# Kernel tuning notes

Measured on AMD Instinct MI355X. Metric: run time of the kernel, lower is better.

## Reference

```python
import jax, jax.numpy as jnp
import numpy as np

D_MODEL = 2048
D_STATE = 64
D_CONV = 4
EXPAND = 2
HEADDIM = 64
NGROUPS = 1
CHUNK = 64
D_INNER = EXPAND * D_MODEL            # 4096
NHEADS = D_INNER // HEADDIM           # 64
D_XBC = D_INNER + 2 * NGROUPS * D_STATE
D_IN_PROJ = 2 * D_INNER + 2 * NGROUPS * D_STATE + NHEADS


def setup_inputs():
    key = jax.random.key(0)
    ks = jax.random.split(key, 8)
    B, L = 2, 4096
    u = jax.random.normal(ks[0], (B, L, D_MODEL), jnp.float32)
    W_in = jax.random.normal(ks[1], (D_IN_PROJ, D_MODEL), jnp.float32) * 0.02
    conv_w = jax.random.normal(ks[2], (D_XBC, D_CONV), jnp.float32) * 0.2
    conv_b = jnp.zeros((D_XBC,), jnp.float32)
    dt = jnp.exp(jax.random.uniform(ks[3], (NHEADS,)) * (np.log(0.1) - np.log(0.001)) + np.log(0.001))
    dt = jnp.clip(dt, 1e-4)
    dt_bias = dt + jnp.log(-jnp.expm1(-dt))
    A_log = jnp.log(jax.random.uniform(ks[4], (NHEADS,), minval=1.0, maxval=16.0))
    D_param = jnp.ones((NHEADS,), jnp.float32)
    norm_w = jnp.ones((D_INNER,), jnp.float32)
    W_out = jax.random.normal(ks[5], (D_MODEL, D_INNER), jnp.float32) * 0.02
    return dict(u=u, W_in=W_in, conv_w=conv_w, conv_b=conv_b, dt_bias=dt_bias,
                A_log=A_log, D_param=D_param, norm_w=norm_w, W_out=W_out)


def segsum(x):
    # x: (..., T) -> (..., T, T) with entry [l,s] = sum_{s< i <= l} x[i], -inf above diag
    T = x.shape[-1]
    mask_strict = jnp.tril(jnp.ones((T, T), bool), k=-1)
    mask_incl = jnp.tril(jnp.ones((T, T), bool), k=0)
    xe = jnp.where(mask_strict, x[..., :, None], 0.0)  # element [l,s] = x[l] if l>s
    xseg = jnp.cumsum(xe, axis=-2)
    return jnp.where(mask_incl, xseg, -jnp.inf)


def ssd_scan(X, A, Bm, Cm, block_len=CHUNK):
    # X: (b,L,h,p), A: (b,L,h), Bm/Cm: (b,L,h,n)
    b, seqlen, h, p = X.shape
    n = Bm.shape[-1]
    pad_len = (block_len - seqlen % block_len) % block_len
    if pad_len > 0:
        X = jnp.pad(X, ((0, 0), (0, pad_len), (0, 0), (0, 0)))
        A = jnp.pad(A, ((0, 0), (0, pad_len), (0, 0)))
        Bm = jnp.pad(Bm, ((0, 0), (0, pad_len), (0, 0), (0, 0)))
        Cm = jnp.pad(Cm, ((0, 0), (0, pad_len), (0, 0), (0, 0)))
    L = X.shape[1]
    c = L // block_len
    Xc = X.reshape(b, c, block_len, h, p)
    Ac = A.reshape(b, c, block_len, h).transpose(0, 3, 1, 2)  # (b,h,c,l)
    Bc = Bm.reshape(b, c, block_len, h, n)
    Cc = Cm.reshape(b, c, block_len, h, n)
    A_cum = jnp.cumsum(Ac, axis=-1)                           # (b,h,c,l)
    Lmat = jnp.exp(segsum(Ac))                                # (b,h,c,l,s)
    CB = jnp.einsum('bclhn,bcshn->bhcls', Cc, Bc)
    Y_diag = jnp.einsum('bhcls,bcshp->bhclp', CB * Lmat, Xc)
    decay_states = jnp.exp(A_cum[..., -1:] - A_cum)           # (b,h,c,l)
    states = jnp.einsum('bhcl,bclhn,bclhp->bhcpn', decay_states, Bc, Xc)
    init = jnp.zeros((b, h, 1, p, n), X.dtype)
    states = jnp.concatenate([init, states], axis=2)          # (b,h,c+1,p,n)
    chunk_decay = jnp.pad(A_cum[..., -1], ((0, 0), (0, 0), (1, 0)))  # (b,h,c+1)
    decay_chunk = jnp.exp(segsum(chunk_decay))                # (b,h,c+1,c+1)
    new_states = jnp.einsum('bhzc,bhcpn->bhzpn', decay_chunk, states)[:, :, :-1]
    Y_off = jnp.einsum('bclhn,bhcpn,bhcl->bhclp', Cc, new_states, jnp.exp(A_cum))
    Y = (Y_diag + Y_off).transpose(0, 2, 3, 1, 4).reshape(b, L, h, p)
    if pad_len > 0:
        Y = Y[:, :seqlen]
    return Y


def rmsnorm_grouped(x, w, ngroups, eps=1e-5):
    gs = x.shape[-1] // ngroups
    xg = x.reshape(*x.shape[:-1], ngroups, gs)
    xg = xg * jax.lax.rsqrt(jnp.mean(xg * xg, axis=-1, keepdims=True) + eps)
    return xg.reshape(x.shape) * w


def reference(u, W_in, conv_w, conv_b, dt_bias, A_log, D_param, norm_w, W_out):
    B, L, _ = u.shape
    zxbcdt = u @ W_in.T                                      # (B,L,d_in_proj)
    z = zxbcdt[..., :D_INNER]
    xBC = zxbcdt[..., D_INNER:D_INNER + D_XBC]
    dt = zxbcdt[..., D_INNER + D_XBC:]
    # causal depthwise conv1d, kernel D_CONV, left-pad D_CONV-1
    xpad = jnp.pad(xBC, ((0, 0), (D_CONV - 1, 0), (0, 0)))
    conv = conv_b
    for k in range(D_CONV):
        conv = conv + conv_w[:, k] * xpad[:, k:k + L, :]
    xBC = jax.nn.silu(conv)
    x = xBC[..., :D_INNER].reshape(B, L, NHEADS, HEADDIM)
    B_ssm = xBC[..., D_INNER:D_INNER + NGROUPS * D_STATE].reshape(B, L, NGROUPS, D_STATE)
    C_ssm = xBC[..., D_INNER + NGROUPS * D_STATE:].reshape(B, L, NGROUPS, D_STATE)
    if NGROUPS < NHEADS:
        rep = NHEADS // NGROUPS
        B_ssm = jnp.repeat(B_ssm, rep, axis=2)
        C_ssm = jnp.repeat(C_ssm, rep, axis=2)
    dt = jax.nn.softplus(dt + dt_bias)                        # (B,L,nheads)
    A = -jnp.exp(A_log)                                       # (nheads,)
    y = ssd_scan(x * dt[..., None], A * dt, B_ssm, C_ssm, block_len=CHUNK)
    y = y + D_param[:, None] * x
    y = y.reshape(B, L, D_INNER)
    y = rmsnorm_grouped(y * jax.nn.silu(z), norm_w, NGROUPS)
    return y @ W_out.T
```

## Files before the change

kernel.cpp:

```cpp
#include <hip/hip_runtime.h>
#include <hip/hip_bf16.h>
#include <math.h>

#define SEQ       4096
#define DMODEL    2048
#define DINNER    4096
#define DXBC      4224
#define NPROJ     8384
#define NHEADS    64
#define HDIM      64
#define DSTATE    64
#define NCHUNK    64
#define XLD       4352

typedef __attribute__((ext_vector_type(8))) _Float16 half8;
typedef __attribute__((ext_vector_type(2))) _Float16 half2v;
typedef __attribute__((ext_vector_type(4))) float floatx4;

__device__ __forceinline__ void async_copy16(void* lds, const void* g) {
  __builtin_amdgcn_global_load_lds(
      (const __attribute__((address_space(1))) unsigned int*)g,
      (__attribute__((address_space(3))) unsigned int*)lds, 16, 0, 0);
}

__device__ __forceinline__ float silu_f(float x) { return x / (1.f + __expf(-x)); }

__device__ __forceinline__ void cvt8(const float* __restrict__ s, _Float16* __restrict__ d) {
  float4 a = *(const float4*)s;
  float4 b = *(const float4*)(s + 4);
  half8 h;
  h[0] = (_Float16)a.x; h[1] = (_Float16)a.y; h[2] = (_Float16)a.z; h[3] = (_Float16)a.w;
  h[4] = (_Float16)b.x; h[5] = (_Float16)b.y; h[6] = (_Float16)b.z; h[7] = (_Float16)b.w;
  *(half8*)d = h;
}

__global__ void diag_kernel(float* out, float v) { out[0] = v; }

__global__ void cvt8_kernel(const float* __restrict__ src, _Float16* __restrict__ dst, int n8) {
  int i = blockIdx.x * 256 + threadIdx.x;
  if (i < n8) cvt8(src + (size_t)i * 8, dst + (size_t)i * 8);
}

#define U_N8 (SEQ * DMODEL / 8)
__global__ void cvt_in_kernel(const float* __restrict__ u, const float* __restrict__ W_in,
                              _Float16* __restrict__ ubf, _Float16* __restrict__ winbf) {
  int i = blockIdx.x * 256 + threadIdx.x;
  if (i < U_N8) {
    cvt8(u + (size_t)i * 8, ubf + (size_t)i * 8);
  } else {
    int j = i - U_N8;
    int row = j >> 8;
    size_t off = (size_t)j * 8;
    if (row < NPROJ) {
      cvt8(W_in + off, winbf + off);
    } else {
      half8 zz = {};
      *(half8*)(winbf + off) = zz;
    }
  }
}

template <typename OT>
__global__ __launch_bounds__(256) void gemm_bt64(
    const _Float16* __restrict__ A, const _Float16* __restrict__ B,
    OT* __restrict__ C0, OT* __restrict__ C1, int K,
    int ldc0, int ldc1, int ncol0, int tiles_m, int tiles_n) {
  __shared__ __align__(16) _Float16 As[128 * 64];
  __shared__ __align__(16) _Float16 Bs[128 * 64];
  int t = threadIdx.x;
  int nt = tiles_m * tiles_n;
  int id = blockIdx.x;
  int id2 = ((nt & 7) == 0) ? ((id & 7) * (nt >> 3) + (id >> 3)) : id;
  int wband = tiles_m << 2;
  int g = id2 / wband;
  int rm = id2 - g * wband;
  int bw = tiles_n - (g << 2); if (bw > 4) bw = 4;
  int pn = (g << 2) + rm % bw;
  int pm = rm / bw;
  int m0 = pm * 128, n0 = pn * 128;

  int w = t >> 6, lane = t & 63, q = lane >> 4, r = lane & 15;
  int wm = (w >> 1) * 64, wn = (w & 1) * 64;
  int rowoff = lane >> 3;
  int chunkoff = ((lane & 7) ^ rowoff) * 8;
  const _Float16* gA[4];
  const _Float16* gB[4];
#pragma unroll
  for (int i = 0; i < 4; ++i) {
    gA[i] = A + (size_t)(m0 + i * 32 + w * 8 + rowoff) * K + chunkoff;
    gB[i] = B + (size_t)(n0 + i * 32 + w * 8 + rowoff) * K + chunkoff;
  }
  floatx4 acc[4][4] = {};
  for (int k0 = 0; k0 < K; k0 += 64) {
#pragma unroll
    for (int i = 0; i < 4; ++i) {
      async_copy16(As + (i * 32 + w * 8) * 64, gA[i] + k0);
      async_copy16(Bs + (i * 32 + w * 8) * 64, gB[i] + k0);
    }
    __syncthreads();
#pragma unroll
    for (int kk = 0; kk < 64; kk += 32) {
      half8 af[4], bf[4];
#pragma unroll
      for (int im = 0; im < 4; ++im) {
        int R = wm + im * 16 + r;
        af[im] = *(const half8*)&As[R * 64 + ((((kk >> 3) + q) ^ (R & 7)) << 3)];
      }
#pragma unroll
      for (int in = 0; in < 4; ++in) {
        int R = wn + in * 16 + r;
        bf[in] = *(const half8*)&Bs[R * 64 + ((((kk >> 3) + q) ^ (R & 7)) << 3)];
      }
#pragma unroll
      for (int im = 0; im < 4; ++im)
#pragma unroll
        for (int in = 0; in < 4; ++in)
          acc[im][in] =
              __builtin_amdgcn_mfma_f32_16x16x32_f16(af[im], bf[in], acc[im][in], 0, 0, 0);
    }
    __syncthreads();
  }
  OT* Cp = (n0 < ncol0) ? C0 : C1;
  int ldc = (n0 < ncol0) ? ldc0 : ldc1;
  int cb = (n0 < ncol0) ? n0 : n0 - ncol0;
#pragma unroll
  for (int im = 0; im < 4; ++im)
#pragma unroll
    for (int in = 0; in < 4; ++in)
#pragma unroll
      for (int i = 0; i < 4; ++i)
        Cp[(size_t)(m0 + wm + im * 16 + q * 4 + i) * ldc + cb + wn + in * 16 + r] =
            (OT)acc[im][in][i];
}

template <typename OT>
__global__ __launch_bounds__(512, 2) void gemm256(
    const _Float16* __restrict__ A, const _Float16* __restrict__ B,
    OT* __restrict__ C, int K, int ldc, int tiles_m, int tiles_n) {
  __shared__ __align__(16) _Float16 As[2][2][128 * 64];
  __shared__ __align__(16) _Float16 Bs[2][2][128 * 64];
  int t = threadIdx.x;
  int nwg = tiles_m * tiles_n;
  int id = blockIdx.x;
  int wgid = ((nwg & 7) == 0) ? ((id & 7) * (nwg >> 3) + (id >> 3)) : id;
  int wband = tiles_m << 2;
  int g = wgid / wband;
  int rm = wgid - g * wband;
  int bw = tiles_n - (g << 2); if (bw > 4) bw = 4;
  int pn = (g << 2) + rm % bw;
  int pm = rm / bw;
  int m0 = pm * 256, n0 = pn * 256;

  int w = t >> 6, lane = t & 63, q4 = lane >> 4, r16 = lane & 15;
  int srow = lane >> 3;
  int schunk = ((lane & 7) ^ srow) << 3;
  const _Float16* gAb = A + (size_t)(m0 + w * 8 + srow) * K + schunk;
  const _Float16* gBb = B + (size_t)(n0 + w * 8 + srow) * K + schunk;
  int Ra = (w >> 2) * 64 + r16;
  int Rb = (w & 3) * 32 + r16;

  floatx4 acc[4][4][2] = {};
  half8 af[4][2], bf[2][2];

#define STAGE_A(buf_, H_, kt_)                                                 \
  {                                                                            \
    _Pragma("unroll") for (int i_ = 0; i_ < 2; ++i_)                           \
        async_copy16(&As[buf_][H_][(i_ * 64 + w * 8) * 64],                    \
                     gAb + (size_t)((H_)*128 + i_ * 64) * K + ((kt_) << 6));   \
  }
#define STAGE_B(buf_, H_, kt_)                                                 \
  {                                                                            \
    _Pragma("unroll") for (int i_ = 0; i_ < 2; ++i_)                           \
        async_copy16(&Bs[buf_][H_][(i_ * 64 + w * 8) * 64],                    \
                     gBb + (size_t)((H_)*128 + i_ * 64) * K + ((kt_) << 6));   \
  }
#define LDA(half_)                                                             \
  _Pragma("unroll") for (int m_ = 0; m_ < 4; ++m_)                             \
  _Pragma("unroll") for (int k_ = 0; k_ < 2; ++k_) {                           \
    int R_ = Ra + m_ * 16;                                                     \
    af[m_][k_] = *(const half8*)&As[cur][half_]                                \
        [R_ * 64 + (((k_ * 4 + q4) ^ (R_ & 7)) << 3)];                         \
  }
#define LDB(half_)                                                             \
  _Pragma("unroll") for (int n_ = 0; n_ < 2; ++n_)                             \
  _Pragma("unroll") for (int k_ = 0; k_ < 2; ++k_) {                           \
    int R_ = Rb + n_ * 16;                                                     \
    bf[n_][k_] = *(const half8*)&Bs[cur][half_]                                \
        [R_ * 64 + (((k_ * 4 + q4) ^ (R_ & 7)) << 3)];                         \
  }
#define MM(sq_)                                                                \
  __builtin_amdgcn_s_setprio(1);                                               \
  _Pragma("unroll") for (int m_ = 0; m_ < 4; ++m_)                             \
  _Pragma("unroll") for (int n_ = 0; n_ < 2; ++n_)                             \
  _Pragma("unroll") for (int k_ = 0; k_ < 2; ++k_)                             \
      acc[sq_][m_][n_] = __builtin_amdgcn_mfma_f32_16x16x32_f16(               \
          af[m_][k_], bf[n_][k_], acc[sq_][m_][n_], 0, 0, 0);                  \
  __builtin_amdgcn_s_setprio(0);
#define BARF() { __builtin_amdgcn_s_barrier(); asm volatile("" ::: "memory"); }
#define WAITLGKM()                                                             \
  {                                                                            \
    asm volatile("s_waitcnt lgkmcnt(0)" ::: "memory");                         \
    __builtin_amdgcn_sched_barrier(0);                                         \
  }

  int NT = K >> 6;
  STAGE_A(0, 0, 0);
  STAGE_B(0, 0, 0);
  STAGE_B(0, 1, 0);
  STAGE_A(0, 1, 0);
  asm volatile("s_waitcnt vmcnt(2)" ::: "memory");
  BARF();

  for (int kt = 0; kt < NT; ++kt) {
    int cur = kt & 1, nxt = cur ^ 1;
    bool more = (kt + 1 < NT);
    LDA(0);
    LDB(0);
    if (more) STAGE_A(nxt, 0, kt + 1);
    BARF();
    WAITLGKM();
    MM(0);
    BARF();
    LDB(1);
    if (more) {
      STAGE_B(nxt, 0, kt + 1);
      asm volatile("s_waitcnt vmcnt(4)" ::: "memory");
    } else {
      asm volatile("s_waitcnt vmcnt(0)" ::: "memory");
    }
    BARF();
    WAITLGKM();
    MM(1);
    BARF();
    LDA(1);
    if (more) STAGE_B(nxt, 1, kt + 1);
    BARF();
    WAITLGKM();
    MM(2);
    BARF();
    LDB(0);
    if (more) {
      STAGE_A(nxt, 1, kt + 1);
      asm volatile("s_waitcnt vmcnt(2)" ::: "memory");
    }
    BARF();
    WAITLGKM();
    MM(3);
    BARF();
  }

  const int paC[4] = {0, 0, 1, 1};
  const int pbC[4] = {0, 1, 1, 0};
#pragma unroll
  for (int sq = 0; sq < 4; ++sq) {
    int rb = m0 + paC[sq] * 128 + (w >> 2) * 64 + q4 * 4;
    int cb = n0 + pbC[sq] * 128 + (w & 3) * 32 + r16;
#pragma unroll
    for (int m = 0; m < 4; ++m)
#pragma unroll
      for (int n = 0; n < 2; ++n)
#pragma unroll
        for (int i = 0; i < 4; ++i)
          C[(size_t)(rb + m * 16 + i) * ldc + cb + n * 16] = (OT)acc[sq][m][n][i];
  }
#undef STAGE_A
#undef STAGE_B
#undef LDA
#undef LDB
#undef MM
#undef BARF
#undef WAITLGKM
}

#define CONVB (SEQ * (DXBC / 2) / 256)
__global__ __launch_bounds__(256) void conv_dtscan_kernel(
    const _Float16* __restrict__ xin, const float* __restrict__ conv_w,
    const float* __restrict__ conv_b, _Float16* __restrict__ xcv,
    const float* __restrict__ dt_bias, const float* __restrict__ A_log,
    float* __restrict__ dtp, float* __restrict__ acum, float* __restrict__ chs) {
  int t = threadIdx.x;
  if (blockIdx.x < CONVB) {
    int idx = blockIdx.x * 256 + t;
    int l = idx / (DXBC / 2);
    int c = (idx - l * (DXBC / 2)) * 2;
    const _Float16* zc = xin + (size_t)l * XLD + c;
    float a0 = conv_b[c], a1 = conv_b[c + 1];
#pragma unroll
    for (int k = 0; k < 4; ++k) {
      int off = k - 3;
      if (l + off >= 0) {
        half2v v = *(const half2v*)(zc + (long)off * XLD);
        a0 += conv_w[c * 4 + k] * (float)v[0];
        a1 += conv_w[c * 4 + 4 + k] * (float)v[1];
      }
    }
    half2v o;
    o[0] = (_Float16)silu_f(a0);
    o[1] = (_Float16)silu_f(a1);
    *(half2v*)(xcv + (size_t)l * DXBC + c) = o;
  } else {
    __shared__ float dAs[64 * 65];
    int c = blockIdx.x - CONVB;
    int h = t & 63;
    const _Float16* dtraw = xin + DXBC;
    float bias = dt_bias[h];
    float negA = -__expf(A_log[h]);
#pragma unroll
    for (int i = 0; i < 16; ++i) {
      int l = i * 4 + (t >> 6);
      int row = c * 64 + l;
      float x = (float)dtraw[(size_t)row * XLD + h] + bias;
      float dtv = (x > 20.f) ? x : log1pf(__expf(x));
      dtp[(size_t)row * 64 + h] = dtv;
      dAs[l * 65 + h] = negA * dtv;
    }
    __syncthreads();
    if (t < 64) {
      float a = 0.f;
      size_t base = ((size_t)c * 64 + t) * 64;
      for (int l = 0; l < 64; ++l) {
        a += dAs[l * 65 + t];
        acum[base + l] = a;
      }
      chs[c * 64 + t] = a;
    }
  }
}

__global__ __launch_bounds__(256) void states_kernel(
    const _Float16* __restrict__ xcv, const float* __restrict__ dtp,
    const float* __restrict__ acum, const float* __restrict__ chs,
    _Float16* __restrict__ states) {
  int bid = blockIdx.x;
  int c = bid & 63, h = bid >> 6;
  int row0 = c * 64;
  int acbase = (c * 64 + h) * 64;
  __shared__ __align__(16) _Float16 XdT[64 * 72];
  __shared__ __align__(16) _Float16 BdT[64 * 72];
  __shared__ float dec[64];
  int t = threadIdx.x;
  if (t < 64) dec[t] = __expf(chs[acbase >> 6] - acum[acbase + t]);
  __syncthreads();
#pragma unroll
  for (int i = 0; i < 16; ++i) {
    int flat = i * 256 + t;
    int l = flat >> 6, col = flat & 63;
    int grow = row0 + l;
    float dtv = dtp[(size_t)grow * 64 + h];
    float xv = (float)xcv[(size_t)grow * DXBC + h * 64 + col] * dtv;
    XdT[col * 72 + l] = (_Float16)xv;
    float bv = (float)xcv[(size_t)grow * DXBC + DINNER + col] * dec[l];
    BdT[col * 72 + l] = (_Float16)bv;
  }
  __syncthreads();
  int w = t >> 6, lane = t & 63, q = lane >> 4, r = lane & 15;
#pragma unroll
  for (int in = 0; in < 4; ++in) {
    floatx4 a4 = {0.f, 0.f, 0.f, 0.f};
#pragma unroll
    for (int k0 = 0; k0 < 64; k0 += 32) {
      half8 af = *(const half8*)&XdT[(w * 16 + r) * 72 + k0 + q * 8];
      half8 bf = *(const half8*)&BdT[(in * 16 + r) * 72 + k0 + q * 8];
      a4 = __builtin_amdgcn_mfma_f32_16x16x32_f16(af, bf, a4, 0, 0, 0);
    }
#pragma unroll
    for (int i = 0; i < 4; ++i)
      states[((size_t)bid * 64 + (w * 16 + q * 4 + i)) * 64 + in * 16 + r] = (_Float16)a4[i];
  }
}

__global__ __launch_bounds__(256) void scan_kernel(_Float16* __restrict__ states,
                                                   const float* __restrict__ chs) {
  int bid = blockIdx.x;
  int h = bid >> 4, seg = bid & 15;
  size_t base = ((size_t)h * 64) * 4096 + seg * 256 + threadIdx.x;
  float carry = 0.f;
  float s_cur = (float)states[base];
  for (int c = 0; c < 64; ++c) {
    size_t idx = base + (size_t)c * 4096;
    float s_next = (c < 63) ? (float)states[idx + 4096] : 0.f;
    float ec = __expf(chs[c * 64 + h]);
    states[idx] = (_Float16)carry;
    carry = carry * ec + s_cur;
    s_cur = s_next;
  }
}

__global__ __launch_bounds__(256) void yout_kernel(
    const _Float16* __restrict__ xcv, const float* __restrict__ dtp,
    const float* __restrict__ acum, const _Float16* __restrict__ sin_,
    const float* __restrict__ Dp, _Float16* __restrict__ Y) {
  int bid = blockIdx.x;
  int c = bid & 63, h = bid >> 6;
  int row0 = c * 64;
  int acbase = (c * 64 + h) * 64;
  __shared__ __align__(16) _Float16 Cs[64 * 72];
  __shared__ __align__(16) _Float16 Bt[64 * 72];
  __shared__ __align__(16) _Float16 XdT[64 * 72];
  __shared__ __align__(16) _Float16 Ms[64 * 72];
  __shared__ float acs[64];
  int t = threadIdx.x;
  if (t < 64) acs[t] = acum[acbase + t];
#pragma unroll
  for (int i = 0; i < 16; ++i) {
    int flat = i * 256 + t;
    int l = flat >> 6, col = flat & 63;
    int grow = row0 + l;
    const _Float16* rp = xcv + (size_t)grow * DXBC;
    Cs[l * 72 + col] = rp[DINNER + DSTATE + col];
    Bt[l * 72 + col] = rp[DINNER + col];
    float xv = (float)rp[h * 64 + col] * dtp[(size_t)grow * 64 + h];
    XdT[col * 72 + l] = (_Float16)xv;
  }
  __syncthreads();
  int w = t >> 6, lane = t & 63, q = lane >> 4, r = lane & 15;
  int m = w * 16 + r;
#pragma unroll
  for (int in = 0; in < 4; ++in) {
    floatx4 cb = {0.f, 0.f, 0.f, 0.f};
#pragma unroll
    for (int k0 = 0; k0 < 64; k0 += 32) {
      half8 af = *(const half8*)&Cs[m * 72 + k0 + q * 8];
      half8 bf = *(const half8*)&Bt[(in * 16 + r) * 72 + k0 + q * 8];
      cb = __builtin_amdgcn_mfma_f32_16x16x32_f16(af, bf, cb, 0, 0, 0);
    }
#pragma unroll
    for (int i = 0; i < 4; ++i) {
      int l = w * 16 + q * 4 + i;
      int s = in * 16 + r;
      float v = (s <= l) ? cb[i] * __expf(acs[l] - acs[s]) : 0.f;
      Ms[l * 72 + s] = (_Float16)v;
    }
  }
  __syncthreads();
  size_t sbase = (size_t)bid * 4096;
  float Dh = Dp[h];
#pragma unroll
  for (int in = 0; in < 4; ++in) {
    floatx4 acc = {0.f, 0.f, 0.f, 0.f};
#pragma unroll
    for (int k0 = 0; k0 < 64; k0 += 32) {
      half8 af = *(const half8*)&Cs[m * 72 + k0 + q * 8];
      half8 bf = *(const half8*)&sin_[sbase + (size_t)(in * 16 + r) * 64 + k0 + q * 8];
      acc = __builtin_amdgcn_mfma_f32_16x16x32_f16(af, bf, acc, 0, 0, 0);
    }
#pragma unroll
    for (int i = 0; i < 4; ++i) acc[i] *= __expf(acs[w * 16 + q * 4 + i]);
#pragma unroll
    for (int k0 = 0; k0 < 64; k0 += 32) {
      half8 af = *(const half8*)&Ms[m * 72 + k0 + q * 8];
      half8 bf = *(const half8*)&XdT[(in * 16 + r) * 72 + k0 + q * 8];
      acc = __builtin_amdgcn_mfma_f32_16x16x32_f16(af, bf, acc, 0, 0, 0);
    }
#pragma unroll
    for (int i = 0; i < 4; ++i) {
      int l = w * 16 + q * 4 + i;
      int p = in * 16 + r;
      int grow = row0 + l;
      float xv = (float)xcv[(size_t)grow * DXBC + h * 64 + p];
      Y[(size_t)grow * DINNER + h * 64 + p] = (_Float16)(acc[i] + Dh * xv);
    }
  }
}

__global__ __launch_bounds__(256) void rmsnorm_kernel(const _Float16* __restrict__ Y,
                                                      _Float16* __restrict__ Z,
                                                      const float* __restrict__ norm_w) {
  int row = blockIdx.x;
  const half8* y8 = (const half8*)(Y + (size_t)row * DINNER);
  half8* z8 = (half8*)(Z + (size_t)row * DINNER);
  __shared__ float red[4];
  int t = threadIdx.x;
  float g[16];
  float ss = 0.f;
#pragma unroll
  for (int i = 0; i < 2; ++i) {
    int j = i * 256 + t;
    half8 yv = y8[j];
    half8 zv = z8[j];
#pragma unroll
    for (int e = 0; e < 8; ++e) {
      float gv = (float)yv[e] * silu_f((float)zv[e]);
      g[i * 8 + e] = gv;
      ss += gv * gv;
    }
  }
#pragma unroll
  for (int o = 32; o > 0; o >>= 1) ss += __shfl_down(ss, o, 64);
  if ((t & 63) == 0) red[t >> 6] = ss;
  __syncthreads();
  float rs = rsqrtf((red[0] + red[1] + red[2] + red[3]) / (float)DINNER + 1e-5f);
#pragma unroll
  for (int i = 0; i < 2; ++i) {
    int j = i * 256 + t;
    const float4* w4 = (const float4*)(norm_w + j * 8);
    float4 wa = w4[0], wb = w4[1];
    half8 o;
    o[0] = (_Float16)(g[i * 8 + 0] * rs * wa.x);
    o[1] = (_Float16)(g[i * 8 + 1] * rs * wa.y);
    o[2] = (_Float16)(g[i * 8 + 2] * rs * wa.z);
    o[3] = (_Float16)(g[i * 8 + 3] * rs * wa.w);
    o[4] = (_Float16)(g[i * 8 + 4] * rs * wb.x);
    o[5] = (_Float16)(g[i * 8 + 5] * rs * wb.y);
    o[6] = (_Float16)(g[i * 8 + 6] * rs * wb.z);
    o[7] = (_Float16)(g[i * 8 + 7] * rs * wb.w);
    z8[j] = o;
  }
}

extern "C" void kernel_launch(void* const* d_in, const int* in_sizes, int n_in,
                              void* d_out, int out_size, void* d_ws, size_t ws_size,
                              hipStream_t stream) {
  const float* u       = (const float*)d_in[0];
  const float* W_in    = (const float*)d_in[1];
  const float* conv_w  = (const float*)d_in[2];
  const float* conv_b  = (const float*)d_in[3];
  const float* dt_bias = (const float*)d_in[4];
  const float* A_log   = (const float*)d_in[5];
  const float* D_param = (const float*)d_in[6];
  const float* norm_w  = (const float*)d_in[7];
  const float* W_out   = (const float*)d_in[8];
  float* out = (float*)d_out;
  char* ws = (char*)d_ws;

  const size_t NEED_MID   = 192954368ULL;
  const size_t NEED_SMALL = 140525568ULL;
  bool big = (ws_size >= NEED_MID);
  if (!big && ws_size < NEED_SMALL) {
    diag_kernel<<<1, 1, 0, stream>>>(out, (float)ws_size);
    return;
  }

  if (big) {
    _Float16* zb     = (_Float16*)(ws + 0);
    _Float16* xbcdtb = (_Float16*)(ws + 67108864ULL);
    _Float16* xcv    = (_Float16*)(ws + 102760448ULL);
    _Float16* winbf  = xcv;
    _Float16* states = (_Float16*)(ws + 137363456ULL);
    _Float16* ubf    = states;
    _Float16* woutbf = (_Float16*)(ws + 170917888ULL);
    float* dtp  = (float*)(ws + 187695104ULL);
    float* acum = (float*)(ws + 188743680ULL);
    float* chs  = (float*)(ws + 189792256ULL);

    cvt8_kernel<<<DMODEL * DINNER / 8 / 256, 256, 0, stream>>>(
        W_out, woutbf, DMODEL * DINNER / 8);

    for (int b = 0; b < 2; ++b) {
      const float* ub = u + (size_t)b * SEQ * DMODEL;
      _Float16* zbb = zb + (size_t)b * SEQ * DINNER;

      cvt_in_kernel<<<U_N8 / 256 + 8448, 256, 0, stream>>>(ub, W_in, ubf, winbf);

      gemm256<_Float16><<<256, 512, 0, stream>>>(ubf, winbf, zbb, DMODEL, DINNER, 16, 16);
      gemm_bt64<_Float16><<<32 * 34, 256, 0, stream>>>(
          ubf, winbf + (size_t)DINNER * DMODEL, xbcdtb, xbcdtb,
          DMODEL, XLD, XLD, 1 << 30, 32, 34);

      conv_dtscan_kernel<<<CONVB + NCHUNK, 256, 0, stream>>>(
          xbcdtb, conv_w, conv_b, xcv, dt_bias, A_log, dtp, acum, chs);

      states_kernel<<<NHEADS * NCHUNK, 256, 0, stream>>>(xcv, dtp, acum, chs, states);
      scan_kernel<<<NHEADS * 16, 256, 0, stream>>>(states, chs);
      yout_kernel<<<NHEADS * NCHUNK, 256, 0, stream>>>(xcv, dtp, acum, states, D_param,
                                                       xbcdtb );

      rmsnorm_kernel<<<SEQ, 256, 0, stream>>>(xbcdtb, zbb, norm_w);
    }

    gemm256<float><<<256, 512, 0, stream>>>(zb, woutbf, out, DINNER, DMODEL, 32, 8);
  } else {
    _Float16* zb     = (_Float16*)(ws + 0);
    _Float16* xbcdtb = (_Float16*)(ws + 33554432ULL);
    _Float16* Yb     = xbcdtb;
    _Float16* xcv    = (_Float16*)(ws + 69206016ULL);
    _Float16* winbf  = xcv;
    _Float16* states = (_Float16*)(ws + 103809024ULL);
    _Float16* ubf    = states;
    _Float16* woutbf = states;
    float* dtp  = (float*)(ws + 137363456ULL);
    float* acum = (float*)(ws + 139460608ULL);
    float* chs  = (float*)(ws + 140509184ULL);

    for (int b = 0; b < 2; ++b) {
      const float* ub = u + (size_t)b * SEQ * DMODEL;
      float* outb = out + (size_t)b * SEQ * DMODEL;

      cvt_in_kernel<<<U_N8 / 256 + 8448, 256, 0, stream>>>(ub, W_in, ubf, winbf);
      gemm_bt64<_Float16><<<32 * 66, 256, 0, stream>>>(
          ubf, winbf, zb, xbcdtb, DMODEL, DINNER, XLD, DINNER, 32, 66);
      conv_dtscan_kernel<<<CONVB + NCHUNK, 256, 0, stream>>>(
          xbcdtb, conv_w, conv_b, xcv, dt_bias, A_log, dtp, acum, chs);
      states_kernel<<<NHEADS * NCHUNK, 256, 0, stream>>>(xcv, dtp, acum, chs, states);
      scan_kernel<<<NHEADS * 16, 256, 0, stream>>>(states, chs);
      yout_kernel<<<NHEADS * NCHUNK, 256, 0, stream>>>(xcv, dtp, acum, states, D_param, Yb);
      rmsnorm_kernel<<<SEQ, 256, 0, stream>>>(Yb, zb, norm_w);
      cvt8_kernel<<<DMODEL * DINNER / 8 / 256, 256, 0, stream>>>(
          W_out, woutbf, DMODEL * DINNER / 8);
      gemm_bt64<float><<<32 * 16, 256, 0, stream>>>(
          zb, woutbf, outb, outb, DINNER, DMODEL, DMODEL, 1 << 30, 32, 16);
    }
  }
}
```

Before: 1.092 ms.

## Deepen gemm256 prefetch to two k-tiles and fold xBC projection into it

The 256x256 GEMM now stages loads two k-iterations ahead instead of one, reusing the current buffer once its sub-tiles have been consumed. Its vmcnt waits move to the end of each iteration. The kernel also gains a split output (C0/C1 by column), so the in-projection GEMM covers both the z columns and the first 4096 xBC columns in a single 512-workgroup launch. Only the small 128-column tail (B/C/dt) is left to the 64-tile kernel. The goal is to hide global-load latency better and to run most of the projection on the faster large-tile kernel, at the cost of more in-flight loads and subtler buffer-reuse hazards.

```diff
diff --git a/kernel.cpp b/kernel.cpp
--- a/kernel.cpp
+++ b/kernel.cpp
@@ -136,7 +136,8 @@
 template <typename OT>
 __global__ __launch_bounds__(512, 2) void gemm256(
     const _Float16* __restrict__ A, const _Float16* __restrict__ B,
-    OT* __restrict__ C, int K, int ldc, int tiles_m, int tiles_n) {
+    OT* __restrict__ C0, OT* __restrict__ C1, int K,
+    int ldc0, int ldc1, int ncol0, int tiles_m, int tiles_n) {
   __shared__ __align__(16) _Float16 As[2][2][128 * 64];
   __shared__ __align__(16) _Float16 Bs[2][2][128 * 64];
   int t = threadIdx.x;
@@ -205,63 +206,71 @@
 
   int NT = K >> 6;
   STAGE_A(0, 0, 0);
-  STAGE_B(0, 0, 0);
   STAGE_B(0, 1, 0);
   STAGE_A(0, 1, 0);
-  asm volatile("s_waitcnt vmcnt(2)" ::: "memory");
+  STAGE_B(0, 0, 0);
+  if (NT > 1) {
+    STAGE_A(1, 0, 1);
+    STAGE_B(1, 1, 1);
+    STAGE_A(1, 1, 1);
+    asm volatile("s_waitcnt vmcnt(6)" ::: "memory");
+  } else {
+    asm volatile("s_waitcnt vmcnt(0)" ::: "memory");
+  }
   BARF();
 
   for (int kt = 0; kt < NT; ++kt) {
     int cur = kt & 1, nxt = cur ^ 1;
-    bool more = (kt + 1 < NT);
     LDA(0);
     LDB(0);
-    if (more) STAGE_A(nxt, 0, kt + 1);
+    if (kt + 1 < NT) STAGE_B(nxt, 0, kt + 1);
     BARF();
     WAITLGKM();
     MM(0);
     BARF();
     LDB(1);
-    if (more) {
-      STAGE_B(nxt, 0, kt + 1);
-      asm volatile("s_waitcnt vmcnt(4)" ::: "memory");
-    } else {
-      asm volatile("s_waitcnt vmcnt(0)" ::: "memory");
-    }
+    if (kt + 2 < NT) STAGE_A(cur, 0, kt + 2);
     BARF();
     WAITLGKM();
     MM(1);
     BARF();
     LDA(1);
-    if (more) STAGE_B(nxt, 1, kt + 1);
+    if (kt + 2 < NT) STAGE_B(cur, 1, kt + 2);
     BARF();
     WAITLGKM();
     MM(2);
     BARF();
     LDB(0);
-    if (more) {
-      STAGE_A(nxt, 1, kt + 1);
-      asm volatile("s_waitcnt vmcnt(2)" ::: "memory");
-    }
+    if (kt + 2 < NT) STAGE_A(cur, 1, kt + 2);
     BARF();
     WAITLGKM();
     MM(3);
+    if (kt + 1 < NT) {
+      if (kt + 2 < NT) {
+        asm volatile("s_waitcnt vmcnt(6)" ::: "memory");
+      } else {
+        asm volatile("s_waitcnt vmcnt(0)" ::: "memory");
+      }
+    }
     BARF();
   }
 
   const int paC[4] = {0, 0, 1, 1};
   const int pbC[4] = {0, 1, 1, 0};
+  OT* Cp = (n0 < ncol0) ? C0 : C1;
+  int ldc = (n0 < ncol0) ? ldc0 : ldc1;
+  int cb0 = (n0 < ncol0) ? n0 : n0 - ncol0;
 #pragma unroll
   for (int sq = 0; sq < 4; ++sq) {
     int rb = m0 + paC[sq] * 128 + (w >> 2) * 64 + q4 * 4;
-    int cb = n0 + pbC[sq] * 128 + (w & 3) * 32 + r16;
+    int cb = cb0 + pbC[sq] * 128 + (w & 3) * 32 + r16;
 #pragma unroll
     for (int m = 0; m < 4; ++m)
 #pragma unroll
       for (int n = 0; n < 2; ++n)
 #pragma unroll
         for (int i = 0; i < 4; ++i)
-          C[(size_t)(rb + m * 16 + i) * ldc + cb + n * 16] = (OT)acc[sq][m][n][i];
+          Cp[(size_t)(rb + m * 16 + i) * ldc + cb + n * 16] = (OT)acc[sq][m][n][i];
   }
 #undef STAGE_A
 #undef STAGE_B
@@ -552,10 +561,11 @@
 
       cvt_in_kernel<<<U_N8 / 256 + 8448, 256, 0, stream>>>(ub, W_in, ubf, winbf);
 
-      gemm256<_Float16><<<256, 512, 0, stream>>>(ubf, winbf, zbb, DMODEL, DINNER, 16, 16);
-      gemm_bt64<_Float16><<<32 * 34, 256, 0, stream>>>(
-          ubf, winbf + (size_t)DINNER * DMODEL, xbcdtb, xbcdtb,
-          DMODEL, XLD, XLD, 1 << 30, 32, 34);
+      gemm256<_Float16><<<512, 512, 0, stream>>>(
+          ubf, winbf, zbb, xbcdtb, DMODEL, DINNER, XLD, DINNER, 16, 32);
+      gemm_bt64<_Float16><<<64, 256, 0, stream>>>(
+          ubf, winbf + (size_t)2 * DINNER * DMODEL, xbcdtb + DINNER, xbcdtb + DINNER,
+          DMODEL, XLD, XLD, 1 << 30, 32, 2);
 
       conv_dtscan_kernel<<<CONVB + NCHUNK, 256, 0, stream>>>(
           xbcdtb, conv_w, conv_b, xcv, dt_bias, A_log, dtp, acum, chs);
@@ -568,7 +578,8 @@
       rmsnorm_kernel<<<SEQ, 256, 0, stream>>>(xbcdtb, zbb, norm_w);
     }
 
-    gemm256<float><<<256, 512, 0, stream>>>(zb, woutbf, out, DINNER, DMODEL, 32, 8);
+    gemm256<float><<<256, 512, 0, stream>>>(
+        zb, woutbf, out, out, DINNER, DMODEL, DMODEL, 1 << 30, 32, 8);
   } else {
     _Float16* zb     = (_Float16*)(ws + 0);
     _Float16* xbcdtb = (_Float16*)(ws + 33554432ULL);
```

Result: no change. 1.100 ms (+0.8%).
